# Kernel optimization log

Hardware: AMD Instinct MI355X
Metric: run time of the kernel (lower is better)

The kernel has to match this reference:

```python
import jax, jax.numpy as jnp
import numpy as np

B, K = 2048, 128
M = 5 * K
ALPHA = 1.0 / K          # alpha_k = 1/K
VARTHETA = 0.1
PMAX = 10.0
BIG = 1e9


def _gnn(HW, X, W0a, W1a, W0b, W1b):
    """Order-1 graph filter GNN (HWGCN, K0=[1,1]): relu hidden layer, linear output.
    HW: (B,K,K), X: (B,K,Fin) -> (B,K,Fout)."""
    SX = jnp.einsum('bij,bjf->bif', HW, X)
    Z = jax.nn.relu(X @ W0a + SX @ W1a)              # (B,K,32)
    SZ = jnp.einsum('bij,bjh->bih', HW, Z)
    return Z @ W0b + SZ @ W1b                        # (B,K,Fout)


def setup_inputs() -> dict:
    key = jax.random.key(0)
    ks = jax.random.split(key, 16)
    s = 0.05
    d = {
        'num_itr': 10,
        'kth': 9,
        'HW': jnp.abs(jax.random.normal(ks[0], (B, K, K), jnp.float32)) * s,
        'x0_tmp': jax.random.uniform(ks[1], (B, M), jnp.float32),
        'nu3_val': jnp.array([0.1], jnp.float32),
        'tilde_gamma_val': jnp.array([2.0], jnp.float32),
        'A9': jax.random.normal(ks[2], (1,), jnp.float32),
        'A1': jax.random.normal(ks[3], (1,), jnp.float32),
        'A3': jax.random.normal(ks[4], (1,), jnp.float32),
        'A7': jax.random.normal(ks[5], (1,), jnp.float32),
        'b7': jax.random.normal(ks[6], (1,), jnp.float32),
        'A10': jax.random.normal(ks[7], (1,), jnp.float32),
        'g1_W0a': jax.random.normal(ks[8], (5, 32), jnp.float32) * s,
        'g1_W1a': jax.random.normal(ks[9], (5, 32), jnp.float32) * s,
        'g1_W0b': jax.random.normal(ks[10], (32, 2), jnp.float32) * s,
        'g1_W1b': jax.random.normal(ks[11], (32, 2), jnp.float32) * s,
        'g2_W0a': jax.random.normal(ks[12], (K + 5, 32), jnp.float32) * s,
        'g2_W1a': jax.random.normal(ks[13], (K + 5, 32), jnp.float32) * s,
        'g2_W0b': jax.random.normal(ks[14], (32, 5), jnp.float32) * s,
        'g2_W1b': jax.random.normal(ks[15], (32, 5), jnp.float32) * s,
    }
    return d


def reference(num_itr, kth, HW, x0_tmp, nu3_val, tilde_gamma_val,
              A9, A1, A3, A7, b7, A10,
              g1_W0a, g1_W1a, g1_W0b, g1_W1b,
              g2_W0a, g2_W1a, g2_W0b, g2_W1b):
    nu3 = nu3_val[0]
    tg = tilde_gamma_val[0]
    x = x0_tmp                                        # (B, 5K)

    # REGNN 1 -> step sizes lbd (B,2)
    X1 = x.reshape(B, 5, K).transpose(0, 2, 1)        # (B,K,5)
    lbd = jax.nn.relu(jnp.mean(_gnn(HW, X1, g1_W0a, g1_W1a, g1_W0b, g1_W1b), axis=1))

    # vectorized per-K gradient steps on segments [K:2K] and [4K:5K]
    s0, s1, s2, s3, s4 = (x[:, i * K:(i + 1) * K] for i in range(5))
    s1 = s1 - lbd[:, 0:1] * (ALPHA / (1.0 + s1))
    s4 = s4 + lbd[:, 1:2] * (ALPHA * VARTHETA)
    x = jnp.concatenate([s0, s1, s2, s3, s4], axis=1)

    # REGNN 2 correction
    X2 = x.reshape(B, 5, K).transpose(0, 2, 1)        # (B,K,5)
    tilde = _gnn(HW, jnp.concatenate([HW, X2], axis=-1),
                 g2_W0a, g2_W1a, g2_W0b, g2_W1b)      # (B,K,5)
    x = x + tilde.transpose(0, 2, 1).reshape(B, M)

    # proj onto C8: sum of first K entries <= Pmax (||q||^2 = K)
    f = jnp.sum(x[:, :K], axis=1) - PMAX              # (B,)
    q = jnp.concatenate([jnp.ones(K, x.dtype), jnp.zeros(4 * K, x.dtype)])
    x = jnp.where((f <= 0)[:, None], x, x - f[:, None] * q / K)

    # banded elementwise box clamps (faithful sequential max/min)
    idx = jnp.arange(M)
    band = lambda a, b: (idx >= a) & (idx < b)
    Vnu = 1.0 - 1.0 / (1.0 + nu3) ** 2
    Vg = 1.0 - 1.0 / (1.0 + tg) ** 2
    x = jnp.maximum(jnp.where(band(K, 2 * K), nu3, 0.0), x)
    x = jnp.minimum(jnp.where(band(2 * K, 3 * K), tg, BIG), x)
    x = jnp.maximum(jnp.where(band(3 * K, 4 * K), Vnu, 0.0), x)
    x = jnp.minimum(jnp.where(band(3 * K, 4 * K), Vg, BIG), x)

    if kth == num_itr - 1:  # static python branch
        x = jnp.maximum(x, 0.0)
        xg = x[:, 2 * K:3 * K]   # gamma
        xv = x[:, 3 * K:4 * K]   # V
        f5 = 1.0 - 1.0 / (1.0 + xg) ** 2 - xv
        f6 = jnp.sqrt(xv) - x[:, 4 * K:5 * K]
        p = x[:, 0:K]
        nu = x[:, K:2 * K]
        diagHW = jnp.diagonal(HW, axis1=1, axis2=2)   # (B,K)
        top = p * diagHW
        down = jnp.einsum('bi,bij->bj', p, HW) - top + 1.0
        f4 = top - down * xg
        f2 = nu * down - top
        return (x, f5, f6, f4, f2)
    return (x,)
```

## Files before the change

kernel.cpp:

```cpp
#include <hip/hip_runtime.h>
#include <math.h>

#define B_N 2048
#define KK 128
#define MM 640
#define HS 136
#define ZSS 40
#define SXS 12
#define ALPHA (1.0f/128.0f)
#define VARTHETA 0.1f
#define PMAXV 10.0f
#define BIGV 1000000000.0f

typedef __attribute__((ext_vector_type(8))) short short8;
typedef __attribute__((ext_vector_type(4))) short short4v;
typedef __attribute__((ext_vector_type(4))) float floatx4;
typedef __attribute__((ext_vector_type(4))) __bf16 bf16x4;

static __device__ __forceinline__ unsigned short f2bf(float f) {
    return __builtin_bit_cast(unsigned short, (__bf16)f);
}
static __device__ __forceinline__ short4v cvt4(floatx4 v) {
    return __builtin_bit_cast(short4v, __builtin_convertvector(v, bf16x4));
}
static __device__ __forceinline__ float bf2f(unsigned short h) {
    unsigned u = ((unsigned)h) << 16;
    return __builtin_bit_cast(float, u);
}
static __device__ __forceinline__ short8 pack8(floatx4 lo, floatx4 hi) {
    short4v a = cvt4(lo), b4 = cvt4(hi);
    return __builtin_shufflevector(a, b4, 0, 1, 2, 3, 4, 5, 6, 7);
}
static __device__ __forceinline__ const float* launder_ptr(const float* p) {
    unsigned long long v = (unsigned long long)p;
    asm volatile("" : "+s"(v));
    return (const float*)v;
}

#define H_W1AT 0
#define H_C2T  8704
#define H_ZBP  17408
#define H_ET   27648
#define H_T0F  29696

__global__ __launch_bounds__(512, 4)
void unfold_pocs_kernel(
    const int* __restrict__ num_itr_p, const int* __restrict__ kth_p,
    const float* __restrict__ HW, const float* __restrict__ x0,
    const float* __restrict__ nu3_p, const float* __restrict__ tg_p,
    const float* __restrict__ g1_W0a, const float* __restrict__ g1_W1a,
    const float* __restrict__ g1_W0b, const float* __restrict__ g1_W1b,
    const float* __restrict__ g2_W0a, const float* __restrict__ g2_W1a,
    const float* __restrict__ g2_W0b, const float* __restrict__ g2_W1b,
    float* __restrict__ out)
{
    __shared__ __align__(16) unsigned char H[KK*HS*2];
    __shared__ __align__(16) float SXs_s[KK*SXS];
    __shared__ __align__(16) float xb[MM];
    __shared__ __align__(16) unsigned short xbf[5*HS];
    __shared__ __align__(16) unsigned short x2bf[KK*8];
    __shared__ __align__(16) unsigned short w1abf[32*8];
    __shared__ __align__(16) unsigned short w0abf[32*8];
    __shared__ __align__(16) float g1w0a[160], g1w1a[160];
    __shared__ __align__(16) float g1w0b[64],  g1w1b[64];
    __shared__ __align__(16) float w0b2[160],  w1b2[160];
    __shared__ float red[16];

    unsigned short* hwb  = (unsigned short*)H;
    unsigned short* w1aT = (unsigned short*)(H + H_W1AT);
    unsigned short* c2T  = (unsigned short*)(H + H_C2T);
    unsigned short* zbp  = (unsigned short*)(H + H_ZBP);
    unsigned short* eT   = (unsigned short*)(H + H_ET);
    float*          t0f  = (float*)(H + H_T0F);
    float*          cw   = (float*)H;
    float*          SXs  = SXs_s;

    const int t = threadIdx.x;
    const int b = blockIdx.x;
    const float* HWb = HW + (size_t)b * (KK*KK);

    const int wv = t >> 6, lane = t & 63, quad = lane >> 4, lr = lane & 15;
    const int arow = wv*16 + lr;

    #pragma unroll
    for (int it = 0; it < 8; ++it) {
        int qi = it * 512 + t;
        int rrow = qi >> 5, q = qi & 31;
        floatx4 v = *(const floatx4*)(HWb + rrow*KK + q*4);
        *(short4v*)&hwb[rrow*HS + q*4] = cvt4(v);
    }
    {
        const int n = (t & 255) >> 3, j = t & 7;
        if (t < 256) w1abf[t]       = (j < 5) ? f2bf(g2_W1a[(KK + j)*32 + n]) : (unsigned short)0;
        else if (t < 512) w0abf[t - 256] = (j < 5) ? f2bf(g2_W0a[(KK + j)*32 + n]) : (unsigned short)0;
    }
    if (t < 160) {
        floatx4 v = *(const floatx4*)(x0 + (size_t)b*MM + t*4);
        *(floatx4*)(xb + t*4) = v;
        *(short4v*)&xbf[(t >> 5)*HS + ((t*4) & 127)] = cvt4(v);
        g1w0a[t] = g1_W0a[t];
        g1w1a[t] = g1_W1a[t];
        w0b2[t]  = g2_W0b[t];
        w1b2[t]  = g2_W1b[t];
    }
    if (t < 64) { g1w0b[t] = g1_W0b[t]; g1w1b[t] = g1_W1b[t]; }
    __syncthreads();

    {
        floatx4 acc = {0.f, 0.f, 0.f, 0.f};
        const int ns = lr < 5 ? lr : 4;
        #pragma unroll
        for (int kt = 0; kt < 4; ++kt) {
            short8 a  = *(const short8*)&hwb[arow*HS + kt*32 + quad*8];
            short8 bb = *(const short8*)&xbf[ns*HS   + kt*32 + quad*8];
            acc = __builtin_amdgcn_mfma_f32_16x16x32_bf16(a, bb, acc, 0, 0, 0);
        }
        if (lr < 5) {
            #pragma unroll
            for (int r = 0; r < 4; ++r)
                SXs[(wv*16 + quad*4 + r)*SXS + lr] = acc[r];
        }
    }
    __syncthreads();

    const int row = t >> 2, g = t & 3;

    short8 A[4];
    {
        float sx[5], x1r[5];
        #pragma unroll
        for (int f = 0; f < 5; ++f) { sx[f] = SXs[row*SXS + f]; x1r[f] = xb[f*KK + row]; }

        float zb0p0=0, zb0p1=0, zb1p0=0, zb1p1=0;
        #pragma unroll
        for (int hh = 0; hh < 8; ++hh) {
            int h = 8*g + hh;
            float a = 0.0f;
            #pragma unroll
            for (int f = 0; f < 5; ++f) a += x1r[f]*g1w0a[f*32+h] + sx[f]*g1w1a[f*32+h];
            a = fmaxf(a, 0.0f);
            zb0p0 += a * g1w0b[h*2+0];
            zb0p1 += a * g1w0b[h*2+1];
            zb1p0 += a * g1w1b[h*2+0];
            zb1p1 += a * g1w1b[h*2+1];
        }
        float mp = 0.0f;
        for (int w = 0; w < 32; ++w) {
            int i = 4*w + g;
            mp += bf2f(hwb[i*HS + row]);
        }
        mp += __shfl_xor(mp, 1); mp += __shfl_xor(mp, 2);
        float m = mp * (1.0f/KK);
        float c0 = zb0p0*(1.0f/KK) + m*zb1p0;
        float c1 = zb0p1*(1.0f/KK) + m*zb1p1;
        #pragma unroll
        for (int s = 1; s < 64; s <<= 1) { c0 += __shfl_xor(c0, s); c1 += __shfl_xor(c1, s); }
        if (lane == 0) { red[wv*2] = c0; red[wv*2 + 1] = c1; }
    }
    #pragma unroll
    for (int kt = 0; kt < 4; ++kt)
        A[kt] = *(const short8*)&hwb[arow*HS + kt*32 + quad*8];
    __syncthreads();

    {
        float lbd0 = 0.f, lbd1 = 0.f;
        #pragma unroll
        for (int w2 = 0; w2 < 8; ++w2) { lbd0 += red[w2*2]; lbd1 += red[w2*2+1]; }
        lbd0 = fmaxf(lbd0, 0.0f); lbd1 = fmaxf(lbd1, 0.0f);

        const int i0 = 2*t, m = i0 >> 3, f0 = i0 & 7;
        float va = (f0     < 5) ? xb[f0*KK + m]     : 0.f;
        float vb = (f0 + 1 < 5) ? xb[(f0+1)*KK + m] : 0.f;
        if (f0 == 0) { vb = vb - lbd0 * (ALPHA / (1.0f + vb)); xb[KK + m]   = vb; }
        if (f0 == 4) { va = va + lbd1 * (ALPHA * VARTHETA);    xb[4*KK + m] = va; }
        ushort2 p; p.x = f2bf(va); p.y = f2bf(vb);
        *(ushort2*)&x2bf[i0] = p;
    }
    {
        const int n = t & 31, seg = t >> 5;
        unsigned short tmp[8];
        #pragma unroll
        for (int i = 0; i < 8; ++i) tmp[i] = f2bf(g2_W1a[(seg*8 + i)*32 + n]);
        *(short8*)&w1aT[n*HS + seg*8] = *(short8*)tmp;
    }
    __syncthreads();

    #pragma unroll
    for (int nt = 0; nt < 2; ++nt) {
        const int n = nt*16 + lr, mmb = wv*16 + quad*4;
        floatx4 acc = {0.f, 0.f, 0.f, 0.f};
        short8 ax2 = {0,0,0,0,0,0,0,0}, bx2 = {0,0,0,0,0,0,0,0};
        if (quad == 0) {
            ax2 = *(const short8*)&x2bf[(wv*16 + lr)*8];
            bx2 = *(const short8*)&w1abf[n*8];
        }
        acc = __builtin_amdgcn_mfma_f32_16x16x32_bf16(ax2, bx2, acc, 0, 0, 0);
        #pragma unroll
        for (int kt = 0; kt < 4; ++kt) {
            short8 bb = *(const short8*)&w1aT[n*HS + kt*32 + quad*8];
            acc = __builtin_amdgcn_mfma_f32_16x16x32_bf16(A[kt], bb, acc, 0, 0, 0);
        }
        ushort4 pe;
        pe.x = f2bf(acc[0] + g2_W0a[(mmb+0)*32 + n]);
        pe.y = f2bf(acc[1] + g2_W0a[(mmb+1)*32 + n]);
        pe.z = f2bf(acc[2] + g2_W0a[(mmb+2)*32 + n]);
        pe.w = f2bf(acc[3] + g2_W0a[(mmb+3)*32 + n]);
        *(ushort4*)&c2T[n*HS + mmb] = pe;
    }
    __syncthreads();

    #pragma unroll
    for (int nt = 0; nt < 2; ++nt) {
        const int n = nt*16 + lr, mmb = wv*16 + quad*4;
        floatx4 acc = {0.f, 0.f, 0.f, 0.f};
        short8 ax2 = {0,0,0,0,0,0,0,0}, bx2 = {0,0,0,0,0,0,0,0};
        if (quad == 0) {
            ax2 = *(const short8*)&x2bf[(wv*16 + lr)*8];
            bx2 = *(const short8*)&w0abf[n*8];
        }
        acc = __builtin_amdgcn_mfma_f32_16x16x32_bf16(ax2, bx2, acc, 0, 0, 0);
        #pragma unroll
        for (int kt = 0; kt < 4; ++kt) {
            short8 bb = *(const short8*)&c2T[n*HS + kt*32 + quad*8];
            acc = __builtin_amdgcn_mfma_f32_16x16x32_bf16(A[kt], bb, acc, 0, 0, 0);
        }
        #pragma unroll
        for (int r = 0; r < 4; ++r)
            zbp[(mmb + r)*ZSS + n] = f2bf(fmaxf(acc[r], 0.0f));
    }
    __syncthreads();

    {
        float ev[5] = {0,0,0,0,0}, t0v[5] = {0,0,0,0,0};
        short8 zrow = *(const short8*)&zbp[row*ZSS + g*8];
        #pragma unroll
        for (int hh = 0; hh < 8; ++hh) {
            int h = 8*g + hh;
            float zv = bf2f((unsigned short)zrow[hh]);
            #pragma unroll
            for (int c = 0; c < 5; ++c) {
                ev[c]  += zv * w1b2[h*5 + c];
                t0v[c] += zv * w0b2[h*5 + c];
            }
        }
        #pragma unroll
        for (int c = 0; c < 5; ++c) {
            ev[c]  += __shfl_xor(ev[c], 1);  ev[c]  += __shfl_xor(ev[c], 2);
            t0v[c] += __shfl_xor(t0v[c], 1); t0v[c] += __shfl_xor(t0v[c], 2);
        }
        if (g == 0) {
            #pragma unroll
            for (int c = 0; c < 5; ++c) {
                eT[c*HS + row]  = f2bf(ev[c]);
                t0f[row*8 + c]  = t0v[c];
            }
        }
    }
    __syncthreads();

    {
        floatx4 acc = {0.f, 0.f, 0.f, 0.f};
        const int ns = lr < 5 ? lr : 4;
        #pragma unroll
        for (int kt = 0; kt < 4; ++kt) {
            short8 bb = *(const short8*)&eT[ns*HS + kt*32 + quad*8];
            acc = __builtin_amdgcn_mfma_f32_16x16x32_bf16(A[kt], bb, acc, 0, 0, 0);
        }
        if (lr < 5) {
            #pragma unroll
            for (int r = 0; r < 4; ++r) {
                int mm = wv*16 + quad*4 + r;
                xb[lr*KK + mm] += acc[r] + t0f[mm*8 + lr];
            }
        }
    }
    __syncthreads();

    float pv = (t < KK) ? xb[t] : 0.0f;
    #pragma unroll
    for (int s = 1; s < 64; s <<= 1) pv += __shfl_xor(pv, s);
    if (lane == 0) red[wv] = pv;
    __syncthreads();
    float fv = -PMAXV;
    #pragma unroll
    for (int w2 = 0; w2 < 8; ++w2) fv += red[w2];

    const int num_itr = num_itr_p[0], kth = kth_p[0];
    const bool flag = (kth == num_itr - 1);
    const float nu3 = nu3_p[0], tg = tg_p[0];
    const float onu = 1.0f + nu3, otg = 1.0f + tg;
    const float Vnu = 1.0f - 1.0f/(onu*onu), Vg = 1.0f - 1.0f/(otg*otg);
    float* outx = out + (size_t)b * MM;

    #pragma unroll
    for (int r2 = 0; r2 < 2; ++r2) {
        int idx = r2*512 + t;
        if (idx < MM) {
            float v = xb[idx];
            if (idx < KK && fv > 0.0f) v -= fv * (1.0f/KK);
            v = fmaxf(v, (idx >= KK   && idx < 2*KK) ? nu3 : 0.0f);
            v = fminf(v, (idx >= 2*KK && idx < 3*KK) ? tg  : BIGV);
            v = fmaxf(v, (idx >= 3*KK && idx < 4*KK) ? Vnu : 0.0f);
            v = fminf(v, (idx >= 3*KK && idx < 4*KK) ? Vg  : BIGV);
            if (flag) v = fmaxf(v, 0.0f);
            xb[idx] = v;
            outx[idx] = v;
        }
    }

    if (flag) {
        __syncthreads();
        const size_t O1 = (size_t)B_N*MM;
        const size_t OK = (size_t)B_N*KK;
        if (t < KK) {
            float xg = xb[2*KK + t], xv = xb[3*KK + t];
            float u1 = 1.0f + xg;
            out[O1 + (size_t)b*KK + t]      = 1.0f - 1.0f/(u1*u1) - xv;
            out[O1 + OK + (size_t)b*KK + t] = sqrtf(xv) - xb[4*KK + t];
        }
        {
            const float* hwr = launder_ptr(HWb);
            float pval = xb[arow];
            #pragma unroll
            for (int kt = 0; kt < 4; ++kt) {
                const float* arp = hwr + arow*KK + kt*32 + quad*8;
                floatx4 lo = *(const floatx4*)(arp);
                floatx4 hi = *(const floatx4*)(arp + 4);
                short8 ad = pack8(lo, hi);
                float v[8];
                #pragma unroll
                for (int j = 0; j < 8; ++j) v[j] = pval * bf2f((unsigned short)ad[j]);
                #pragma unroll
                for (int s = 1; s < 16; s <<= 1) {
                    #pragma unroll
                    for (int j = 0; j < 8; ++j) v[j] += __shfl_xor(v[j], s);
                }
                if (lr == 0) {
                    #pragma unroll
                    for (int j = 0; j < 8; ++j) cw[wv*KK + kt*32 + quad*8 + j] = v[j];
                }
            }
        }
        __syncthreads();
        if (t < KK) {
            float dp = 0.0f;
            #pragma unroll
            for (int w = 0; w < 8; ++w) dp += cw[w*KK + t];
            float p_  = xb[t], nuv = xb[KK + t], xg = xb[2*KK + t];
            float diag = bf2f(f2bf(HWb[t*KK + t]));
            float top  = p_ * diag;
            float down = dp - top + 1.0f;
            out[O1 + 2*OK + (size_t)b*KK + t] = top - down * xg;
            out[O1 + 3*OK + (size_t)b*KK + t] = nuv * down - top;
        }
    }
}

extern "C" void kernel_launch(void* const* d_in, const int* in_sizes, int n_in,
                              void* d_out, int out_size, void* d_ws, size_t ws_size,
                              hipStream_t stream) {
    unfold_pocs_kernel<<<dim3(B_N), dim3(512), 0, stream>>>(
        (const int*)d_in[0], (const int*)d_in[1],
        (const float*)d_in[2], (const float*)d_in[3],
        (const float*)d_in[4], (const float*)d_in[5],
        (const float*)d_in[12], (const float*)d_in[13],
        (const float*)d_in[14], (const float*)d_in[15],
        (const float*)d_in[16], (const float*)d_in[17],
        (const float*)d_in[18], (const float*)d_in[19],
        (float*)d_out);
}
```

Before: 273.5 us.

## Make HW staging wave-local, drop first block barrier and shuffle SX in registers

Each wave now loads and converts only the 16 HW rows it later consumes, so the first SX MFMA runs without a block-wide barrier (only a scheduling barrier). The X operand is loaded straight from global into registers and packed to bf16, so the xbf staging buffer goes away. SX results move to the row/group layout through lane shuffles instead of an LDS round trip. Shared memory is re-aliased into a separate hwb array plus a smaller slot, freeing LDS, and the W1a transpose is hoisted earlier. In exchange an extra barrier is added before the A fragments are reloaded, and register pressure rises from holding 16 float4 values in flight.

```diff
diff --git a/kernel.cpp b/kernel.cpp
--- a/kernel.cpp
+++ b/kernel.cpp
@@ -6,7 +6,6 @@
 #define MM 640
 #define HS 136
 #define ZSS 40
-#define SXS 12
 #define ALPHA (1.0f/128.0f)
 #define VARTHETA 0.1f
 #define PMAXV 10.0f
@@ -36,12 +35,6 @@
     asm volatile("" : "+s"(v));
     return (const float*)v;
 }
-
-#define H_W1AT 0
-#define H_C2T  8704
-#define H_ZBP  17408
-#define H_ET   27648
-#define H_T0F  29696
 
 __global__ __launch_bounds__(512, 4)
 void unfold_pocs_kernel(
@@ -54,10 +47,9 @@
     const float* __restrict__ g2_W0b, const float* __restrict__ g2_W1b,
     float* __restrict__ out)
 {
-    __shared__ __align__(16) unsigned char H[KK*HS*2];
-    __shared__ __align__(16) float SXs_s[KK*SXS];
+    __shared__ __align__(16) unsigned short hwb[KK*HS];
+    __shared__ __align__(16) unsigned char slotWZ[10240];
     __shared__ __align__(16) float xb[MM];
-    __shared__ __align__(16) unsigned short xbf[5*HS];
     __shared__ __align__(16) unsigned short x2bf[KK*8];
     __shared__ __align__(16) unsigned short w1abf[32*8];
     __shared__ __align__(16) unsigned short w0abf[32*8];
@@ -66,14 +58,12 @@
     __shared__ __align__(16) float w0b2[160],  w1b2[160];
     __shared__ float red[16];
 
-    unsigned short* hwb  = (unsigned short*)H;
-    unsigned short* w1aT = (unsigned short*)(H + H_W1AT);
-    unsigned short* c2T  = (unsigned short*)(H + H_C2T);
-    unsigned short* zbp  = (unsigned short*)(H + H_ZBP);
-    unsigned short* eT   = (unsigned short*)(H + H_ET);
-    float*          t0f  = (float*)(H + H_T0F);
-    float*          cw   = (float*)H;
-    float*          SXs  = SXs_s;
+    unsigned short* w1aT = (unsigned short*)slotWZ;
+    unsigned short* zbp  = (unsigned short*)slotWZ;
+    unsigned short* c2T  = (unsigned short*)hwb;
+    unsigned short* eT   = (unsigned short*)hwb;
+    float*          t0f  = (float*)((unsigned char*)hwb + 2048);
+    float*          cw   = (float*)((unsigned char*)hwb + 8192);
 
     const int t = threadIdx.x;
     const int b = blockIdx.x;
@@ -82,12 +72,35 @@
     const int wv = t >> 6, lane = t & 63, quad = lane >> 4, lr = lane & 15;
     const int arow = wv*16 + lr;
 
+    floatx4 hv[8];
     #pragma unroll
     for (int it = 0; it < 8; ++it) {
-        int qi = it * 512 + t;
-        int rrow = qi >> 5, q = qi & 31;
-        floatx4 v = *(const floatx4*)(HWb + rrow*KK + q*4);
-        *(short4v*)&hwb[rrow*HS + q*4] = cvt4(v);
+        int qi = it*64 + lane;
+        int r = qi >> 5, q = qi & 31;
+        hv[it] = *(const floatx4*)(HWb + (wv*16 + r)*KK + q*4);
+    }
+    const int ns = lr < 5 ? lr : 4;
+    floatx4 bv[8];
+    #pragma unroll
+    for (int kt = 0; kt < 4; ++kt) {
+        const float* xp = x0 + (size_t)b*MM + ns*KK + kt*32 + quad*8;
+        bv[2*kt]   = *(const floatx4*)(xp);
+        bv[2*kt+1] = *(const floatx4*)(xp + 4);
+    }
+    __builtin_amdgcn_sched_barrier(0);
+
+    #pragma unroll
+    for (int it = 0; it < 8; ++it) {
+        int qi = it*64 + lane;
+        int r = qi >> 5, q = qi & 31;
+        *(short4v*)&hwb[(wv*16 + r)*HS + q*4] = cvt4(hv[it]);
+    }
+    {
+        const int n = t & 31, seg = t >> 5;
+        unsigned short tmp[8];
+        #pragma unroll
+        for (int i = 0; i < 8; ++i) tmp[i] = f2bf(g2_W1a[(seg*8 + i)*32 + n]);
+        *(short8*)&w1aT[n*HS + seg*8] = *(short8*)tmp;
     }
     {
         const int n = (t & 255) >> 3, j = t & 7;
@@ -97,39 +110,43 @@
     if (t < 160) {
         floatx4 v = *(const floatx4*)(x0 + (size_t)b*MM + t*4);
         *(floatx4*)(xb + t*4) = v;
-        *(short4v*)&xbf[(t >> 5)*HS + ((t*4) & 127)] = cvt4(v);
         g1w0a[t] = g1_W0a[t];
         g1w1a[t] = g1_W1a[t];
         w0b2[t]  = g2_W0b[t];
         w1b2[t]  = g2_W1b[t];
     }
     if (t < 64) { g1w0b[t] = g1_W0b[t]; g1w1b[t] = g1_W1b[t]; }
-    __syncthreads();
-
-    {
+    __builtin_amdgcn_sched_barrier(0);
+
+    float sx[5] = {0.f, 0.f, 0.f, 0.f, 0.f};
+    {
+        short8 A1[4];
+        #pragma unroll
+        for (int kt = 0; kt < 4; ++kt)
+            A1[kt] = *(const short8*)&hwb[arow*HS + kt*32 + quad*8];
         floatx4 acc = {0.f, 0.f, 0.f, 0.f};
-        const int ns = lr < 5 ? lr : 4;
         #pragma unroll
         for (int kt = 0; kt < 4; ++kt) {
-            short8 a  = *(const short8*)&hwb[arow*HS + kt*32 + quad*8];
-            short8 bb = *(const short8*)&xbf[ns*HS   + kt*32 + quad*8];
-            acc = __builtin_amdgcn_mfma_f32_16x16x32_bf16(a, bb, acc, 0, 0, 0);
-        }
-        if (lr < 5) {
-            #pragma unroll
-            for (int r = 0; r < 4; ++r)
-                SXs[(wv*16 + quad*4 + r)*SXS + lr] = acc[r];
+            short8 bb = pack8(bv[2*kt], bv[2*kt+1]);
+            acc = __builtin_amdgcn_mfma_f32_16x16x32_bf16(A1[kt], bb, acc, 0, 0, 0);
+        }
+        #pragma unroll
+        for (int r = 0; r < 4; ++r) {
+            #pragma unroll
+            for (int f = 0; f < 5; ++f) {
+                float tmp = __shfl(acc[r], (lane & 48) + f);
+                if (((lane >> 2) & 3) == r) sx[f] = tmp;
+            }
         }
     }
     __syncthreads();
 
     const int row = t >> 2, g = t & 3;
 
-    short8 A[4];
-    {
-        float sx[5], x1r[5];
-        #pragma unroll
-        for (int f = 0; f < 5; ++f) { sx[f] = SXs[row*SXS + f]; x1r[f] = xb[f*KK + row]; }
+    {
+        float x1r[5];
+        #pragma unroll
+        for (int f = 0; f < 5; ++f) x1r[f] = xb[f*KK + row];
 
         float zb0p0=0, zb0p1=0, zb1p0=0, zb1p1=0;
         #pragma unroll
@@ -157,9 +174,6 @@
         for (int s = 1; s < 64; s <<= 1) { c0 += __shfl_xor(c0, s); c1 += __shfl_xor(c1, s); }
         if (lane == 0) { red[wv*2] = c0; red[wv*2 + 1] = c1; }
     }
-    #pragma unroll
-    for (int kt = 0; kt < 4; ++kt)
-        A[kt] = *(const short8*)&hwb[arow*HS + kt*32 + quad*8];
     __syncthreads();
 
     {
@@ -176,13 +190,12 @@
         ushort2 p; p.x = f2bf(va); p.y = f2bf(vb);
         *(ushort2*)&x2bf[i0] = p;
     }
-    {
-        const int n = t & 31, seg = t >> 5;
-        unsigned short tmp[8];
-        #pragma unroll
-        for (int i = 0; i < 8; ++i) tmp[i] = f2bf(g2_W1a[(seg*8 + i)*32 + n]);
-        *(short8*)&w1aT[n*HS + seg*8] = *(short8*)tmp;
-    }
+    __syncthreads();
+
+    short8 A[4];
+    #pragma unroll
+    for (int kt = 0; kt < 4; ++kt)
+        A[kt] = *(const short8*)&hwb[arow*HS + kt*32 + quad*8];
     __syncthreads();
 
     #pragma unroll
@@ -260,10 +273,10 @@
 
     {
         floatx4 acc = {0.f, 0.f, 0.f, 0.f};
-        const int ns = lr < 5 ? lr : 4;
+        const int nse = lr < 5 ? lr : 4;
         #pragma unroll
         for (int kt = 0; kt < 4; ++kt) {
-            short8 bb = *(const short8*)&eT[ns*HS + kt*32 + quad*8];
+            short8 bb = *(const short8*)&eT[nse*HS + kt*32 + quad*8];
             acc = __builtin_amdgcn_mfma_f32_16x16x32_bf16(A[kt], bb, acc, 0, 0, 0);
         }
         if (lr < 5) {
```

Measured after the change: 277.9 us. Within noise of the previous version (+1.6%).
